# Performance work log

Hardware: AMD Instinct MI355X
Metric: run time of the kernel (lower is better)

The kernel has to match this reference:

```python
import jax, jax.numpy as jnp
import numpy as np

D_MODEL = 256
D_STATE = 64
D_CONV = 4
EXPAND = 2
HEADDIM = 64
D_INNER = EXPAND * D_MODEL            # 512
NHEADS = D_INNER // HEADDIM           # 8
CONV_DIM = D_INNER + 2 * D_STATE      # 640 (ngroups=1)
BATCH = 8
SEQ = 4096


def setup_inputs() -> dict:
    key = jax.random.key(0)
    ks = jax.random.split(key, 6)
    x = jax.random.normal(ks[0], (BATCH, SEQ, D_MODEL), jnp.float32)
    d_in_proj = 2 * D_INNER + 2 * D_STATE + NHEADS  # 1160
    W_in = jax.random.normal(ks[1], (d_in_proj, D_MODEL), jnp.float32) / np.sqrt(D_MODEL)
    conv_w = jax.random.normal(ks[2], (CONV_DIM, D_CONV), jnp.float32) / np.sqrt(D_CONV)
    conv_b = jnp.zeros((CONV_DIM,), jnp.float32)
    # dt_bias = inverse-softplus of dt sampled log-uniform in [1e-3, 0.1] (mamba_ssm init)
    dt = jnp.exp(jax.random.uniform(ks[3], (NHEADS,), jnp.float32, np.log(1e-3), np.log(0.1)))
    dt_bias = dt + jnp.log(-jnp.expm1(-dt))
    A_log = jnp.log(jax.random.uniform(ks[4], (NHEADS,), jnp.float32, 1.0, 16.0))
    Dp = jnp.ones((NHEADS,), jnp.float32)
    gnorm_w = jnp.ones((D_INNER,), jnp.float32)
    norm_w = jnp.ones((D_MODEL,), jnp.float32)
    W_out = jax.random.normal(ks[5], (D_MODEL, D_INNER), jnp.float32) / np.sqrt(D_INNER)
    return {"x": x, "W_in": W_in, "conv_w": conv_w, "conv_b": conv_b,
            "dt_bias": dt_bias, "A_log": A_log, "Dp": Dp,
            "gnorm_w": gnorm_w, "norm_w": norm_w, "W_out": W_out}


def _rmsnorm(x, w, eps):
    return x * jax.lax.rsqrt(jnp.mean(x * x, axis=-1, keepdims=True) + eps) * w


def reference(x, W_in, conv_w, conv_b, dt_bias, A_log, Dp, gnorm_w, norm_w, W_out):
    Bsz, L, _ = x.shape
    # pre-norm (torch nn.RMSNorm eps=None -> finfo eps)
    xn = _rmsnorm(x, norm_w, jnp.finfo(x.dtype).eps)
    zxbcdt = jnp.einsum('bld,ed->ble', xn, W_in)            # (B,L,1160)
    z = zxbcdt[..., :D_INNER]                               # gate (B,L,512)
    xBC = zxbcdt[..., D_INNER:D_INNER + CONV_DIM]           # (B,L,640)
    dt = zxbcdt[..., -NHEADS:]                              # (B,L,8)
    # causal depthwise conv1d + silu
    xpad = jnp.pad(xBC, ((0, 0), (D_CONV - 1, 0), (0, 0)))
    conv = sum(xpad[:, k:k + L, :] * conv_w[:, k] for k in range(D_CONV)) + conv_b
    xBC = jax.nn.silu(conv)
    xs = xBC[..., :D_INNER].reshape(Bsz, L, NHEADS, HEADDIM)  # (B,L,H,P)
    Bm = xBC[..., D_INNER:D_INNER + D_STATE]                  # (B,L,N)
    Cm = xBC[..., D_INNER + D_STATE:]                         # (B,L,N)
    dt = jax.nn.softplus(dt + dt_bias)                        # (B,L,H)
    dA = jnp.exp(dt * (-jnp.exp(A_log)))                      # (B,L,H)

    def step(state, inp):
        dA_t, dt_t, B_t, C_t, x_t = inp  # (B,H) (B,H) (B,N) (B,N) (B,H,P)
        state = state * dA_t[:, :, None, None] \
            + (dt_t[:, :, None] * x_t)[..., None] * B_t[:, None, None, :]
        y = jnp.einsum('bhpn,bn->bhp', state, C_t)
        return state, y

    init = jnp.zeros((Bsz, NHEADS, HEADDIM, D_STATE), x.dtype)
    tm = lambda a: jnp.moveaxis(a, 1, 0)  # time-major for scan
    _, ys = jax.lax.scan(step, init, (tm(dA), tm(dt), tm(Bm), tm(Cm), tm(xs)))
    y = jnp.moveaxis(ys, 0, 1) + Dp[None, None, :, None] * xs  # skip D term
    y = y.reshape(Bsz, L, D_INNER)
    # gated RMSNorm (norm_before_gate=False): rmsnorm(y * silu(z))
    y = _rmsnorm(y * jax.nn.silu(z), gnorm_w, 1e-5)
    return x + jnp.einsum('ble,de->bld', y, W_out)
```

## Files before the change

kernel.cpp:

```cpp
#include <hip/hip_runtime.h>
#include <math.h>

#define BATCH   8
#define SEQ     4096
#define DMODEL  256
#define DINNER  512
#define DSTATE  64
#define NHEADS  8
#define HEADDIM 64
#define CONVDIM 640
#define DPROJ   1160
#define NROWS   (BATCH*SEQ)
#define CHUNK   64
#define NCHUNK  (SEQ/CHUNK)
#define NPAD    1280
#define LSTR    72

typedef short bf16x8 __attribute__((ext_vector_type(8)));
typedef short short8v __attribute__((ext_vector_type(8)));
typedef float f32x4 __attribute__((ext_vector_type(4)));

__device__ short g_xn[(size_t)NROWS * DMODEL];
__device__ short g_zxb[(size_t)NROWS * DPROJ];
__device__ short g_xbc[(size_t)NROWS * CONVDIM];
__device__ float g_dt[(size_t)NROWS * NHEADS];
__device__ float g_rowss[(size_t)NROWS * NHEADS];
__device__ short g_lstate[(size_t)BATCH * NHEADS * NCHUNK * HEADDIM * DSTATE];
__device__ float g_decayC[BATCH * NHEADS * NCHUNK];
__device__ short g_Winb[(size_t)NPAD * DMODEL];
__device__ short g_Woutb[(size_t)DMODEL * DINNER];

__device__ __forceinline__ short f2bf(float f) {
    unsigned u = __float_as_uint(f);
    u += 0x7fff + ((u >> 16) & 1);
    return (short)(u >> 16);
}
__device__ __forceinline__ float bf2f(short s) {
    return __uint_as_float(((unsigned)(unsigned short)s) << 16);
}

__device__ __forceinline__ void stage16(const void* gsrc, void* ldst) {
    __builtin_amdgcn_global_load_lds(
        (const __attribute__((address_space(1))) void*)gsrc,
        (__attribute__((address_space(3))) void*)ldst, 16, 0, 0);
}

__global__ __launch_bounds__(256) void convert_bf16_kernel(const float* __restrict__ src,
                                                           short* __restrict__ dst,
                                                           int n_valid, int n_total) {
    const int i = blockIdx.x * 256 + threadIdx.x;
    if (i < n_total) dst[i] = (i < n_valid) ? f2bf(src[i]) : (short)0;
}

__global__ __launch_bounds__(256) void convert_wout_kernel(const float* __restrict__ src,
                                                           const float* __restrict__ gw,
                                                           short* __restrict__ dst) {
    const int i = blockIdx.x * 256 + threadIdx.x;
    if (i < DMODEL * DINNER) dst[i] = f2bf(src[i] * gw[i % DINNER]);
}

__global__ __launch_bounds__(256) void rmsnorm_dt_kernel(const float* __restrict__ x,
                                                         const float* __restrict__ w,
                                                         const float* __restrict__ W_in,
                                                         short* __restrict__ xn,
                                                         float* __restrict__ dt) {
    const int row  = blockIdx.x * 4 + (threadIdx.x >> 6);
    const int lane = threadIdx.x & 63;
    const float4 v = *(const float4*)(x + (size_t)row * DMODEL + lane * 4);
    float ss = v.x * v.x + v.y * v.y + v.z * v.z + v.w * v.w;
#pragma unroll
    for (int off = 1; off < 64; off <<= 1) ss += __shfl_xor(ss, off);
    const float rs = rsqrtf(ss * (1.0f / DMODEL) + 1.1920929e-7f);
    const float4 wv = *(const float4*)(w + lane * 4);
    const float4 xn4 = make_float4(v.x * rs * wv.x, v.y * rs * wv.y,
                                   v.z * rs * wv.z, v.w * rs * wv.w);
    short4 o;
    o.x = f2bf(xn4.x); o.y = f2bf(xn4.y); o.z = f2bf(xn4.z); o.w = f2bf(xn4.w);
    *(short4*)(xn + (size_t)row * DMODEL + lane * 4) = o;
#pragma unroll
    for (int h = 0; h < NHEADS; ++h) {
        const float4 ww = *(const float4*)(W_in + (size_t)(DPROJ - NHEADS + h) * DMODEL + lane * 4);
        float p = xn4.x * ww.x + xn4.y * ww.y + xn4.z * ww.z + xn4.w * ww.w;
#pragma unroll
        for (int off = 1; off < 64; off <<= 1) p += __shfl_xor(p, off);
        if (lane == 0) dt[(size_t)row * NHEADS + h] = p;
    }
}

template <bool RES, typename OUT>
__global__ __launch_bounds__(256) void gemm_bf16_nt(const short* __restrict__ A,
                                                    const short* __restrict__ B,
                                                    const float* __restrict__ R,
                                                    const float* __restrict__ RS,
                                                    OUT* __restrict__ C,
                                                    int NX, int M, int N, int K, int LDA) {
    const int L   = blockIdx.x;
    const int xcd = L & 7;
    const int r   = L >> 3;
    const int mstrips_per_xcd = (M / 128) >> 3;
    const int mblk = xcd * mstrips_per_xcd + r / NX;
    const int nblk = r % NX;
    const int m0 = mblk * 128, n0 = nblk * 128;

    __shared__ __align__(16) short Asl[128 * 64];
    __shared__ __align__(16) short Bsl[128 * 64];
    const int tid  = threadIdx.x;
    const int lane = tid & 63;
    const int wid  = tid >> 6;
    const int wrow = (wid >> 1) * 64, wcol = (wid & 1) * 64;

    f32x4 acc[4][4];
#pragma unroll
    for (int m = 0; m < 4; ++m)
#pragma unroll
        for (int n = 0; n < 4; ++n) acc[m][n] = (f32x4)0.f;

    const int wbase = (tid & 0xC0) * 8;

    for (int k0 = 0; k0 < K; k0 += 64) {
#pragma unroll
        for (int rr = 0; rr < 4; ++rr) {
            const int idx = rr * 256 + tid;
            const int row = idx >> 3;
            const int cs  = idx & 7;
            const int ko  = (cs ^ (row & 7)) * 8;
            const int r6  = row & 63;
            const int brow = (row & 64) + (((r6 & 15) << 2) | (r6 >> 4));
            stage16(A + (size_t)(m0 + row) * LDA + k0 + ko, Asl + rr * 2048 + wbase);
            stage16(B + (size_t)(n0 + brow) * K + k0 + ko, Bsl + rr * 2048 + wbase);
        }
        __syncthreads();
#pragma unroll
        for (int ks = 0; ks < 2; ++ks) {
            bf16x8 af[4], bfr[4];
#pragma unroll
            for (int m = 0; m < 4; ++m) {
                const int arow = wrow + m * 16 + (lane & 15);
                const int ch = (ks * 4 + (lane >> 4)) ^ (arow & 7);
                af[m] = *(const bf16x8*)(Asl + arow * 64 + ch * 8);
            }
#pragma unroll
            for (int n = 0; n < 4; ++n) {
                const int brw = wcol + n * 16 + (lane & 15);
                const int ch = (ks * 4 + (lane >> 4)) ^ (brw & 7);
                bfr[n] = *(const bf16x8*)(Bsl + brw * 64 + ch * 8);
            }
#pragma unroll
            for (int m = 0; m < 4; ++m)
#pragma unroll
                for (int n = 0; n < 4; ++n)
                    acc[m][n] = __builtin_amdgcn_mfma_f32_16x16x32_bf16(af[m], bfr[n], acc[m][n], 0, 0, 0);
        }
        __syncthreads();
    }

    const int r0 = (lane >> 4) * 4;
    const int gcol = n0 + wcol + (lane & 15) * 4;
#pragma unroll
    for (int m = 0; m < 4; ++m) {
        const int grow = m0 + wrow + m * 16 + r0;
        if (gcol < N) {
#pragma unroll
            for (int reg = 0; reg < 4; ++reg) {
                if constexpr (sizeof(OUT) == 2) {
                    short4 o;
                    o.x = f2bf(acc[m][0][reg]); o.y = f2bf(acc[m][1][reg]);
                    o.z = f2bf(acc[m][2][reg]); o.w = f2bf(acc[m][3][reg]);
                    *(short4*)(C + (size_t)(grow + reg) * N + gcol) = o;
                } else {
                    f32x4 v;
                    v[0] = acc[m][0][reg]; v[1] = acc[m][1][reg];
                    v[2] = acc[m][2][reg]; v[3] = acc[m][3][reg];
                    if (RES) {
                        const float* rp = RS + (size_t)(grow + reg) * NHEADS;
                        const f32x4 s0 = *(const f32x4*)rp;
                        const f32x4 s1 = *(const f32x4*)(rp + 4);
                        const float sum = s0[0] + s0[1] + s0[2] + s0[3] +
                                          s1[0] + s1[1] + s1[2] + s1[3];
                        const float rsn = rsqrtf(sum * (1.0f / DINNER) + 1e-5f);
                        v *= rsn;
                        v += *(const f32x4*)(R + (size_t)(grow + reg) * N + gcol);
                    }
                    *(f32x4*)(C + (size_t)(grow + reg) * N + gcol) = v;
                }
            }
        }
    }
}

__global__ __launch_bounds__(256) void conv_silu_kernel(const short* __restrict__ zxb,
                                                        const float* __restrict__ cw,
                                                        const float* __restrict__ cb,
                                                        short* __restrict__ xbc) {
    const int idx = blockIdx.x * 256 + threadIdx.x;
    const int c8  = (idx % 80) * 8;
    const int bl0 = (idx / 80) * 8;
    const int l0  = bl0 & (SEQ - 1);
    const short* src = zxb + (size_t)bl0 * DPROJ + DINNER + c8;

    float4 w4[8];
    float bias[8];
#pragma unroll
    for (int j = 0; j < 8; ++j) w4[j] = *(const float4*)(cw + (c8 + j) * 4);
    {
        const float4 b0 = *(const float4*)(cb + c8);
        const float4 b1 = *(const float4*)(cb + c8 + 4);
        bias[0] = b0.x; bias[1] = b0.y; bias[2] = b0.z; bias[3] = b0.w;
        bias[4] = b1.x; bias[5] = b1.y; bias[6] = b1.z; bias[7] = b1.w;
    }

    bf16x8 rowv[11];
#pragma unroll
    for (int m = 0; m < 11; ++m) {
        if (l0 + m - 3 >= 0)
            rowv[m] = *(const bf16x8*)(src + (ptrdiff_t)(m - 3) * DPROJ);
        else
            rowv[m] = (bf16x8)0;
    }

#pragma unroll
    for (int r = 0; r < 8; ++r) {
        float acc[8];
#pragma unroll
        for (int j = 0; j < 8; ++j) acc[j] = bias[j];
#pragma unroll
        for (int k = 0; k < 4; ++k) {
            const bf16x8 tap = rowv[r + k];
#pragma unroll
            for (int j = 0; j < 8; ++j)
                acc[j] = fmaf(bf2f(tap[j]), ((const float*)&w4[j])[k], acc[j]);
        }
        short8v o;
#pragma unroll
        for (int j = 0; j < 8; ++j) {
            const float s = acc[j];
            o[j] = f2bf(s / (1.f + __expf(-s)));
        }
        *(short8v*)(xbc + (size_t)(bl0 + r) * CONVDIM + c8) = o;
    }
}

__global__ __launch_bounds__(256) void chunk_state_mfma(const float* __restrict__ dt,
                                                        const short* __restrict__ xbc,
                                                        const float* __restrict__ dt_bias,
                                                        const float* __restrict__ A_log,
                                                        short* __restrict__ lstate,
                                                        float* __restrict__ decayC) {
    const int bhc = blockIdx.x;
    const int c = bhc & (NCHUNK - 1), bh = bhc >> 6, h = bh & (NHEADS - 1), b = bh >> 3;
    const int tid = threadIdx.x, lane = tid & 63, wid = tid >> 6;
    __shared__ short XT[64 * LSTR];
    __shared__ short BT[64 * LSTR];
    __shared__ float wsh[CHUNK];
    const size_t row0 = (size_t)b * SEQ + (size_t)c * CHUNK;

    const float aneg  = -__expf(A_log[h]);
    const float dbias = dt_bias[h];
    if (tid < 64) {
        const float draw = dt[(row0 + tid) * NHEADS + h] + dbias;
        const float dtv  = (draw > 20.f) ? draw : log1pf(__expf(draw));
        float cum = aneg * dtv;
#pragma unroll
        for (int off = 1; off < 64; off <<= 1) {
            const float nv = __shfl_up(cum, off);
            if (lane >= off) cum += nv;
        }
        const float total = __shfl(cum, 63);
        wsh[tid] = __expf(total - cum) * dtv;
        if (tid == 63) decayC[bhc] = __expf(cum);
    }
    __syncthreads();

#pragma unroll
    for (int r = 0; r < 4; ++r) {
        const int idx  = tid + r * 256;
        const int trow = idx >> 4;
        const int q    = idx & 15;
        const int c4   = q * 4;
        const short* rp = xbc + (row0 + trow) * CONVDIM;
        const short4 xv = *(const short4*)(rp + h * 64 + c4);
        const short4 bv = *(const short4*)(rp + DINNER + c4);
        const float w = wsh[trow];
        XT[(c4 + 0) * LSTR + trow] = xv.x;
        XT[(c4 + 1) * LSTR + trow] = xv.y;
        XT[(c4 + 2) * LSTR + trow] = xv.z;
        XT[(c4 + 3) * LSTR + trow] = xv.w;
        BT[(0 * 16 + q) * LSTR + trow] = f2bf(bf2f(bv.x) * w);
        BT[(1 * 16 + q) * LSTR + trow] = f2bf(bf2f(bv.y) * w);
        BT[(2 * 16 + q) * LSTR + trow] = f2bf(bf2f(bv.z) * w);
        BT[(3 * 16 + q) * LSTR + trow] = f2bf(bf2f(bv.w) * w);
    }
    __syncthreads();

    f32x4 acc[4];
#pragma unroll
    for (int n = 0; n < 4; ++n) acc[n] = (f32x4)0.f;
#pragma unroll
    for (int ks = 0; ks < 2; ++ks) {
        const bf16x8 af = *(const bf16x8*)(XT + (wid * 16 + (lane & 15)) * LSTR + ks * 32 + (lane >> 4) * 8);
#pragma unroll
        for (int n = 0; n < 4; ++n) {
            const bf16x8 bfv = *(const bf16x8*)(BT + (n * 16 + (lane & 15)) * LSTR + ks * 32 + (lane >> 4) * 8);
            acc[n] = __builtin_amdgcn_mfma_f32_16x16x32_bf16(af, bfv, acc[n], 0, 0, 0);
        }
    }
    short* lp = lstate + ((size_t)bhc << 12);
    const int ncol = (lane & 15) * 4;
#pragma unroll
    for (int reg = 0; reg < 4; ++reg) {
        const int p = wid * 16 + (lane >> 4) * 4 + reg;
        short4 o;
        o.x = f2bf(acc[0][reg]); o.y = f2bf(acc[1][reg]);
        o.z = f2bf(acc[2][reg]); o.w = f2bf(acc[3][reg]);
        *(short4*)(lp + p * 64 + ncol) = o;
    }
}

__global__ __launch_bounds__(256) void state_prefix_kernel(short* __restrict__ lstate,
                                                           const float* __restrict__ decayC) {
    const int idx = blockIdx.x * 256 + threadIdx.x;
    const int bh = idx >> 12;
    const int pn = idx & 4095;
    float S = 0.f;
    for (int c = 0; c < NCHUNK; ++c) {
        short* ptr = lstate + (((size_t)bh * NCHUNK + c) << 12) + pn;
        const float l = bf2f(*ptr);
        *ptr = f2bf(S);
        S = fmaf(S, decayC[bh * NCHUNK + c], l);
    }
}

__global__ __launch_bounds__(256) void chunk_scan_mfma(const float* __restrict__ dt,
                                                       short* __restrict__ xbc,
                                                       const short* __restrict__ zxb,
                                                       float* __restrict__ rowss,
                                                       const float* __restrict__ dt_bias,
                                                       const float* __restrict__ A_log,
                                                       const float* __restrict__ Dp,
                                                       const short* __restrict__ lstate) {
    const int bhc = blockIdx.x;
    const int c = bhc & (NCHUNK - 1), bh = bhc >> 6, h = bh & (NHEADS - 1), b = bh >> 3;
    const int tid = threadIdx.x, lane = tid & 63, wid = tid >> 6;
    __shared__ short Bs[64 * LSTR];
    __shared__ short Cs[64 * LSTR];
    __shared__ short XT[64 * LSTR];
    __shared__ short SP[64 * LSTR];
    __shared__ short Ms[64 * LSTR];
    __shared__ float cums[CHUNK];
    __shared__ float dtss[CHUNK];
    const size_t row0 = (size_t)b * SEQ + (size_t)c * CHUNK;

#pragma unroll
    for (int r = 0; r < 4; ++r) {
        const int idx  = tid + r * 256;
        const int trow = idx >> 4;
        const int q    = idx & 15;
        const int c4   = q * 4;
        const short* rp = xbc + (row0 + trow) * CONVDIM;
        const short4 xv = *(const short4*)(rp + h * 64 + c4);
        *(short4*)(Bs + trow * LSTR + c4) = *(const short4*)(rp + DINNER + c4);
        *(short4*)(Cs + trow * LSTR + c4) = *(const short4*)(rp + DINNER + DSTATE + c4);
        XT[(0 * 16 + q) * LSTR + trow] = xv.x;
        XT[(1 * 16 + q) * LSTR + trow] = xv.y;
        XT[(2 * 16 + q) * LSTR + trow] = xv.z;
        XT[(3 * 16 + q) * LSTR + trow] = xv.w;
    }
#pragma unroll
    for (int r = 0; r < 4; ++r) {
        const int idx = tid + r * 256;
        const int p = idx >> 4, n4 = (idx & 15) * 4;
        const int pslot = ((p & 3) << 4) | (p >> 2);
        *(short4*)(SP + pslot * LSTR + n4) =
            *(const short4*)(lstate + ((size_t)bhc << 12) + p * 64 + n4);
    }
    const float aneg  = -__expf(A_log[h]);
    const float dbias = dt_bias[h];
    if (tid < 64) {
        const float draw = dt[(row0 + tid) * NHEADS + h] + dbias;
        const float dtv  = (draw > 20.f) ? draw : log1pf(__expf(draw));
        float cum = aneg * dtv;
#pragma unroll
        for (int off = 1; off < 64; off <<= 1) {
            const float nv = __shfl_up(cum, off);
            if (lane >= off) cum += nv;
        }
        cums[tid] = cum;
        dtss[tid] = dtv;
    }
    __syncthreads();

    f32x4 accG[4];
#pragma unroll
    for (int tf = 0; tf < 4; ++tf) accG[tf] = (f32x4)0.f;
#pragma unroll
    for (int ks = 0; ks < 2; ++ks) {
        const bf16x8 af = *(const bf16x8*)(Cs + (wid * 16 + (lane & 15)) * LSTR + ks * 32 + (lane >> 4) * 8);
#pragma unroll
        for (int tf = 0; tf < 4; ++tf) {
            const bf16x8 bfv = *(const bf16x8*)(Bs + (tf * 16 + (lane & 15)) * LSTR + ks * 32 + (lane >> 4) * 8);
            accG[tf] = __builtin_amdgcn_mfma_f32_16x16x32_bf16(af, bfv, accG[tf], 0, 0, 0);
        }
    }
    const int srow0 = wid * 16 + (lane >> 4) * 4;
#pragma unroll
    for (int tf = 0; tf < 4; ++tf) {
        const int t = tf * 16 + (lane & 15);
        const float ct  = cums[t];
        const float dtt = dtss[t];
#pragma unroll
        for (int reg = 0; reg < 4; ++reg) {
            const int s = srow0 + reg;
            const float m = (t <= s) ? accG[tf][reg] * __expf(cums[s] - ct) * dtt : 0.f;
            Ms[s * LSTR + t] = f2bf(m);
        }
    }
    __syncthreads();

    f32x4 acc1[4], acc2[4];
#pragma unroll
    for (int pf = 0; pf < 4; ++pf) { acc1[pf] = (f32x4)0.f; acc2[pf] = (f32x4)0.f; }
#pragma unroll
    for (int ks = 0; ks < 2; ++ks) {
        const bf16x8 am = *(const bf16x8*)(Ms + (wid * 16 + (lane & 15)) * LSTR + ks * 32 + (lane >> 4) * 8);
        const bf16x8 ac = *(const bf16x8*)(Cs + (wid * 16 + (lane & 15)) * LSTR + ks * 32 + (lane >> 4) * 8);
#pragma unroll
        for (int pf = 0; pf < 4; ++pf) {
            const bf16x8 bx = *(const bf16x8*)(XT + (pf * 16 + (lane & 15)) * LSTR + ks * 32 + (lane >> 4) * 8);
            const bf16x8 bs = *(const bf16x8*)(SP + (pf * 16 + (lane & 15)) * LSTR + ks * 32 + (lane >> 4) * 8);
            acc1[pf] = __builtin_amdgcn_mfma_f32_16x16x32_bf16(am, bx, acc1[pf], 0, 0, 0);
            acc2[pf] = __builtin_amdgcn_mfma_f32_16x16x32_bf16(ac, bs, acc2[pf], 0, 0, 0);
        }
    }
    const float dpv = Dp[h];
    float es[4];
#pragma unroll
    for (int reg = 0; reg < 4; ++reg) es[reg] = __expf(cums[srow0 + reg]);
    const int j = lane & 15;
#pragma unroll
    for (int reg = 0; reg < 4; ++reg) {
        const int s = srow0 + reg;
        const short4 z4 = *(const short4*)(zxb + (row0 + s) * DPROJ + h * 64 + j * 4);
        short4 o;
        float ssq = 0.f;
#pragma unroll
        for (int pf = 0; pf < 4; ++pf) {
            const float xv = bf2f(XT[(pf * 16 + j) * LSTR + s]);
            const float yv = acc1[pf][reg] + es[reg] * acc2[pf][reg] + dpv * xv;
            const float zf = bf2f(((const short*)&z4)[pf]);
            const float v  = yv * zf / (1.f + __expf(-zf));
            ((short*)&o)[pf] = f2bf(v);
            ssq = fmaf(v, v, ssq);
        }
        *(short4*)(xbc + (row0 + s) * CONVDIM + h * 64 + j * 4) = o;
        ssq += __shfl_xor(ssq, 1);
        ssq += __shfl_xor(ssq, 2);
        ssq += __shfl_xor(ssq, 4);
        ssq += __shfl_xor(ssq, 8);
        if (j == 0) rowss[(row0 + s) * NHEADS + h] = ssq;
    }
}

extern "C" void kernel_launch(void* const* d_in, const int* in_sizes, int n_in,
                              void* d_out, int out_size, void* d_ws, size_t ws_size,
                              hipStream_t stream) {
    (void)in_sizes; (void)n_in; (void)out_size; (void)d_ws; (void)ws_size;
    const float* x      = (const float*)d_in[0];
    const float* W_in   = (const float*)d_in[1];
    const float* conv_w = (const float*)d_in[2];
    const float* conv_b = (const float*)d_in[3];
    const float* dt_b   = (const float*)d_in[4];
    const float* A_log  = (const float*)d_in[5];
    const float* Dp     = (const float*)d_in[6];
    const float* g_w    = (const float*)d_in[7];
    const float* n_w    = (const float*)d_in[8];
    const float* W_out  = (const float*)d_in[9];
    float* out = (float*)d_out;

    short *xn, *zxb, *xbc, *winb, *woutb, *lst;
    float *dtv, *dcy, *rss;
    hipGetSymbolAddress((void**)&xn,    HIP_SYMBOL(g_xn));
    hipGetSymbolAddress((void**)&zxb,   HIP_SYMBOL(g_zxb));
    hipGetSymbolAddress((void**)&xbc,   HIP_SYMBOL(g_xbc));
    hipGetSymbolAddress((void**)&dtv,   HIP_SYMBOL(g_dt));
    hipGetSymbolAddress((void**)&rss,   HIP_SYMBOL(g_rowss));
    hipGetSymbolAddress((void**)&lst,   HIP_SYMBOL(g_lstate));
    hipGetSymbolAddress((void**)&dcy,   HIP_SYMBOL(g_decayC));
    hipGetSymbolAddress((void**)&winb,  HIP_SYMBOL(g_Winb));
    hipGetSymbolAddress((void**)&woutb, HIP_SYMBOL(g_Woutb));

    convert_bf16_kernel<<<(NPAD * DMODEL) / 256, 256, 0, stream>>>(
        W_in, winb, DPROJ * DMODEL, NPAD * DMODEL);
    convert_wout_kernel<<<(DMODEL * DINNER) / 256, 256, 0, stream>>>(W_out, g_w, woutb);

    rmsnorm_dt_kernel<<<NROWS / 4, 256, 0, stream>>>(x, n_w, W_in, xn, dtv);

    gemm_bf16_nt<false, short><<<(NPAD / 128) * (NROWS / 128), 256, 0, stream>>>(
        xn, winb, nullptr, nullptr, zxb, NPAD / 128, NROWS, DPROJ, DMODEL, DMODEL);

    conv_silu_kernel<<<(NROWS / 8 * 80) / 256, 256, 0, stream>>>(zxb, conv_w, conv_b, xbc);

    chunk_state_mfma<<<BATCH * NHEADS * NCHUNK, 256, 0, stream>>>(dtv, xbc, dt_b, A_log, lst, dcy);
    state_prefix_kernel<<<(BATCH * NHEADS * HEADDIM * DSTATE) / 256, 256, 0, stream>>>(lst, dcy);
    chunk_scan_mfma<<<BATCH * NHEADS * NCHUNK, 256, 0, stream>>>(
        dtv, xbc, zxb, rss, dt_b, A_log, Dp, lst);

    gemm_bf16_nt<true, float><<<(DMODEL / 128) * (NROWS / 128), 256, 0, stream>>>(
        xbc, woutb, x, rss, out, DMODEL / 128, NROWS, DMODEL, DINNER, CONVDIM);
}
```

Before: 188.4 us.

## Trim in_proj GEMM to 1152 columns, vectorize state prefix, alias scan LDS buffers

The in_proj GEMM now computes only the first 1152 output columns (z and xBC) instead of 1280 padded ones, and the zxb buffer stride shrinks to match. The dt columns are already produced by the rmsnorm_dt kernel, so the extra GEMM tiles were wasted work. The state prefix kernel now has each thread handle four contiguous state elements with short4 loads, which cuts the thread count and makes memory accesses wider. The chunk-state kernel permutes the P index for its LDS and global writes, and the chunk-scan kernel reuses one LDS buffer for B and M behind an extra barrier to lower shared-memory use and possibly raise occupancy.

```diff
diff --git a/kernel.cpp b/kernel.cpp
--- a/kernel.cpp
+++ b/kernel.cpp
@@ -10,10 +10,10 @@
 #define HEADDIM 64
 #define CONVDIM 640
 #define DPROJ   1160
+#define ZSTR    1152
 #define NROWS   (BATCH*SEQ)
 #define CHUNK   64
 #define NCHUNK  (SEQ/CHUNK)
-#define NPAD    1280
 #define LSTR    72
 
 typedef short bf16x8 __attribute__((ext_vector_type(8)));
@@ -21,13 +21,13 @@
 typedef float f32x4 __attribute__((ext_vector_type(4)));
 
 __device__ short g_xn[(size_t)NROWS * DMODEL];
-__device__ short g_zxb[(size_t)NROWS * DPROJ];
+__device__ short g_zxb[(size_t)NROWS * ZSTR];
 __device__ short g_xbc[(size_t)NROWS * CONVDIM];
 __device__ float g_dt[(size_t)NROWS * NHEADS];
 __device__ float g_rowss[(size_t)NROWS * NHEADS];
 __device__ short g_lstate[(size_t)BATCH * NHEADS * NCHUNK * HEADDIM * DSTATE];
 __device__ float g_decayC[BATCH * NHEADS * NCHUNK];
-__device__ short g_Winb[(size_t)NPAD * DMODEL];
+__device__ short g_Winb[(size_t)ZSTR * DMODEL];
 __device__ short g_Woutb[(size_t)DMODEL * DINNER];
 
 __device__ __forceinline__ short f2bf(float f) {
@@ -196,7 +196,7 @@
     const int c8  = (idx % 80) * 8;
     const int bl0 = (idx / 80) * 8;
     const int l0  = bl0 & (SEQ - 1);
-    const short* src = zxb + (size_t)bl0 * DPROJ + DINNER + c8;
+    const short* src = zxb + (size_t)bl0 * ZSTR + DINNER + c8;
 
     float4 w4[8];
     float bias[8];
@@ -213,7 +213,7 @@
 #pragma unroll
     for (int m = 0; m < 11; ++m) {
         if (l0 + m - 3 >= 0)
-            rowv[m] = *(const bf16x8*)(src + (ptrdiff_t)(m - 3) * DPROJ);
+            rowv[m] = *(const bf16x8*)(src + (ptrdiff_t)(m - 3) * ZSTR);
         else
             rowv[m] = (bf16x8)0;
     }
@@ -281,10 +281,10 @@
         const short4 xv = *(const short4*)(rp + h * 64 + c4);
         const short4 bv = *(const short4*)(rp + DINNER + c4);
         const float w = wsh[trow];
-        XT[(c4 + 0) * LSTR + trow] = xv.x;
-        XT[(c4 + 1) * LSTR + trow] = xv.y;
-        XT[(c4 + 2) * LSTR + trow] = xv.z;
-        XT[(c4 + 3) * LSTR + trow] = xv.w;
+        XT[(0 * 16 + q) * LSTR + trow] = xv.x;
+        XT[(1 * 16 + q) * LSTR + trow] = xv.y;
+        XT[(2 * 16 + q) * LSTR + trow] = xv.z;
+        XT[(3 * 16 + q) * LSTR + trow] = xv.w;
         BT[(0 * 16 + q) * LSTR + trow] = f2bf(bf2f(bv.x) * w);
         BT[(1 * 16 + q) * LSTR + trow] = f2bf(bf2f(bv.y) * w);
         BT[(2 * 16 + q) * LSTR + trow] = f2bf(bf2f(bv.z) * w);
@@ -305,10 +305,11 @@
         }
     }
     short* lp = lstate + ((size_t)bhc << 12);
+    const int hi = lane >> 4;
     const int ncol = (lane & 15) * 4;
 #pragma unroll
     for (int reg = 0; reg < 4; ++reg) {
-        const int p = wid * 16 + (lane >> 4) * 4 + reg;
+        const int p = 16 * hi + 4 * reg + wid;
         short4 o;
         o.x = f2bf(acc[0][reg]); o.y = f2bf(acc[1][reg]);
         o.z = f2bf(acc[2][reg]); o.w = f2bf(acc[3][reg]);
@@ -319,14 +320,20 @@
 __global__ __launch_bounds__(256) void state_prefix_kernel(short* __restrict__ lstate,
                                                            const float* __restrict__ decayC) {
     const int idx = blockIdx.x * 256 + threadIdx.x;
-    const int bh = idx >> 12;
-    const int pn = idx & 4095;
-    float S = 0.f;
+    const int bh  = idx >> 10;
+    const int pn4 = (idx & 1023) * 4;
+    float S0 = 0.f, S1 = 0.f, S2 = 0.f, S3 = 0.f;
     for (int c = 0; c < NCHUNK; ++c) {
-        short* ptr = lstate + (((size_t)bh * NCHUNK + c) << 12) + pn;
-        const float l = bf2f(*ptr);
-        *ptr = f2bf(S);
-        S = fmaf(S, decayC[bh * NCHUNK + c], l);
+        short4* ptr = (short4*)(lstate + (((size_t)bh * NCHUNK + c) << 12) + pn4);
+        const short4 l4 = *ptr;
+        short4 o;
+        o.x = f2bf(S0); o.y = f2bf(S1); o.z = f2bf(S2); o.w = f2bf(S3);
+        *ptr = o;
+        const float d = decayC[bh * NCHUNK + c];
+        S0 = fmaf(S0, d, bf2f(l4.x));
+        S1 = fmaf(S1, d, bf2f(l4.y));
+        S2 = fmaf(S2, d, bf2f(l4.z));
+        S3 = fmaf(S3, d, bf2f(l4.w));
     }
 }
 
@@ -341,13 +348,14 @@
     const int bhc = blockIdx.x;
     const int c = bhc & (NCHUNK - 1), bh = bhc >> 6, h = bh & (NHEADS - 1), b = bh >> 3;
     const int tid = threadIdx.x, lane = tid & 63, wid = tid >> 6;
-    __shared__ short Bs[64 * LSTR];
+    __shared__ short BsMs[64 * LSTR];
     __shared__ short Cs[64 * LSTR];
     __shared__ short XT[64 * LSTR];
     __shared__ short SP[64 * LSTR];
-    __shared__ short Ms[64 * LSTR];
     __shared__ float cums[CHUNK];
     __shared__ float dtss[CHUNK];
+    short* Bs = BsMs;
+    short* Ms = BsMs;
     const size_t row0 = (size_t)b * SEQ + (size_t)c * CHUNK;
 
 #pragma unroll
@@ -401,6 +409,8 @@
             accG[tf] = __builtin_amdgcn_mfma_f32_16x16x32_bf16(af, bfv, accG[tf], 0, 0, 0);
         }
     }
+    __syncthreads();
+
     const int srow0 = wid * 16 + (lane >> 4) * 4;
 #pragma unroll
     for (int tf = 0; tf < 4; ++tf) {
@@ -439,7 +449,7 @@
 #pragma unroll
     for (int reg = 0; reg < 4; ++reg) {
         const int s = srow0 + reg;
-        const short4 z4 = *(const short4*)(zxb + (row0 + s) * DPROJ + h * 64 + j * 4);
+        const short4 z4 = *(const short4*)(zxb + (row0 + s) * ZSTR + h * 64 + j * 4);
         short4 o;
         float ssq = 0.f;
 #pragma unroll
@@ -488,19 +498,19 @@
     hipGetSymbolAddress((void**)&winb,  HIP_SYMBOL(g_Winb));
     hipGetSymbolAddress((void**)&woutb, HIP_SYMBOL(g_Woutb));
 
-    convert_bf16_kernel<<<(NPAD * DMODEL) / 256, 256, 0, stream>>>(
-        W_in, winb, DPROJ * DMODEL, NPAD * DMODEL);
+    convert_bf16_kernel<<<(ZSTR * DMODEL) / 256, 256, 0, stream>>>(
+        W_in, winb, ZSTR * DMODEL, ZSTR * DMODEL);
     convert_wout_kernel<<<(DMODEL * DINNER) / 256, 256, 0, stream>>>(W_out, g_w, woutb);
 
     rmsnorm_dt_kernel<<<NROWS / 4, 256, 0, stream>>>(x, n_w, W_in, xn, dtv);
 
-    gemm_bf16_nt<false, short><<<(NPAD / 128) * (NROWS / 128), 256, 0, stream>>>(
-        xn, winb, nullptr, nullptr, zxb, NPAD / 128, NROWS, DPROJ, DMODEL, DMODEL);
+    gemm_bf16_nt<false, short><<<(ZSTR / 128) * (NROWS / 128), 256, 0, stream>>>(
+        xn, winb, nullptr, nullptr, zxb, ZSTR / 128, NROWS, ZSTR, DMODEL, DMODEL);
 
     conv_silu_kernel<<<(NROWS / 8 * 80) / 256, 256, 0, stream>>>(zxb, conv_w, conv_b, xbc);
 
     chunk_state_mfma<<<BATCH * NHEADS * NCHUNK, 256, 0, stream>>>(dtv, xbc, dt_b, A_log, lst, dcy);
-    state_prefix_kernel<<<(BATCH * NHEADS * HEADDIM * DSTATE) / 256, 256, 0, stream>>>(lst, dcy);
+    state_prefix_kernel<<<(BATCH * NHEADS * HEADDIM * DSTATE) / (4 * 256), 256, 0, stream>>>(lst, dcy);
     chunk_scan_mfma<<<BATCH * NHEADS * NCHUNK, 256, 0, stream>>>(
         dtv, xbc, zxb, rss, dt_b, A_log, Dp, lst);
 
```

Measured after the change: 174.8 us. -7.2%, faster.
